# Kernel tuning notes

Hardware: AMD Instinct MI355X
Metric: run time of the kernel (lower is better)

## Reference

```python
import jax, jax.numpy as jnp
import numpy as np

T, IN, H, OUT, L = 2048, 128, 128, 128, 2


def setup_inputs() -> dict:
    key = jax.random.key(0)
    ks = jax.random.split(key, 12)
    s_in = 1.0 / np.sqrt(IN)
    s_h = 1.0 / np.sqrt(H)
    s_ff = 1.0 / np.sqrt(2 * H)
    return {
        "emb": jax.random.normal(ks[0], (T, IN), jnp.float32),
        "start": jax.random.randint(ks[1], (T,), 0, 2).astype(jnp.int32),
        "w_in": jax.random.normal(ks[2], (H, IN), jnp.float32) * s_in,
        "b_in": jnp.zeros((H,), jnp.float32),
        "w_out": jax.random.normal(ks[3], (OUT, H), jnp.float32) * s_h,
        "b_out": jnp.zeros((OUT,), jnp.float32),
        "w_f": jax.random.normal(ks[4], (L, 1, H), jnp.float32) * s_h,
        "b_f": jnp.zeros((L, 1), jnp.float32),
        "w_i": jax.random.normal(ks[5], (L, 1, H), jnp.float32) * s_h,
        "b_i": jnp.zeros((L, 1), jnp.float32),
        "w_v": jax.random.normal(ks[6], (L, H, H), jnp.float32) * s_h,
        "b_v": jnp.zeros((L, H), jnp.float32),
        "w_q": jax.random.normal(ks[7], (L, H, H), jnp.float32) * s_h,
        "b_q": jnp.zeros((L, H), jnp.float32),
        "w_k": jax.random.normal(ks[8], (L, H, H), jnp.float32) * s_h,
        "b_k": jnp.zeros((L, H), jnp.float32),
        "w_o": jax.random.normal(ks[9], (L, H, H), jnp.float32) * s_h,
        "b_o": jnp.zeros((L, H), jnp.float32),
        "w_ff": jax.random.normal(ks[10], (L, H, 2 * H), jnp.float32) * s_ff,
        "b_ff": jnp.zeros((L, H), jnp.float32),
    }


def _mlstm_layer(x, gate_mask, w_f, b_f, w_i, b_i, w_v, b_v, w_q, b_q, w_k, b_k, w_o, b_o):
    # x: [T, H] layer input; gate_mask: [T] (0.0 at episode starts -> reset)
    Hdim = x.shape[-1]
    i = jnp.exp(x @ w_i.T + b_i)                           # [T, 1] exp input gate
    v = x @ w_v.T + b_v                                    # [T, H]
    k = (x * (1.0 / np.sqrt(Hdim))) @ w_k.T + b_k          # [T, H] (1/sqrt(H) applied before Linear)
    C = i[:, :, None] * (v[:, :, None] * k[:, None, :])    # [T, H, H] gated outer products
    n = i * k                                              # [T, H]
    g = jax.nn.sigmoid(x @ w_f.T + b_f)[:, 0] * gate_mask  # [T] forget gate, zeroed at resets

    def step(carry, inp):
        S, m = carry
        Ct, nt, gt = inp
        S = gt * S + Ct
        m = gt * m + nt
        return (S, m), (S, m)

    init = (jnp.zeros((Hdim, Hdim), x.dtype), jnp.zeros((Hdim,), x.dtype))
    _, (S_all, m_all) = jax.lax.scan(step, init, (C, n, g))  # [T,H,H], [T,H]

    q = x @ w_q.T + b_q                                    # [T, H]
    o = jax.nn.sigmoid(x @ w_o.T + b_o)                    # [T, H]
    num = jnp.einsum('thk,tk->th', S_all, q)               # C @ q per step
    den = jnp.maximum(jnp.abs(jnp.einsum('th,th->t', m_all, q))[:, None], 1.0)
    return o * (num / den)


def reference(emb, start, w_in, b_in, w_out, b_out, w_f, b_f, w_i, b_i,
              w_v, b_v, w_q, b_q, w_k, b_k, w_o, b_o, w_ff, b_ff):
    gate_mask = 1.0 - start.astype(emb.dtype)              # reset => discard previous state
    e = emb @ w_in.T + b_in                                # [T, H]
    z = e
    for l in range(w_f.shape[0]):
        h = _mlstm_layer(z, gate_mask, w_f[l], b_f[l], w_i[l], b_i[l],
                         w_v[l], b_v[l], w_q[l], b_q[l], w_k[l], b_k[l], w_o[l], b_o[l])
        z = jax.nn.leaky_relu(jnp.concatenate([h, e], axis=-1) @ w_ff[l].T + b_ff[l])
    return z @ w_out.T + b_out
```

## Files before the change

kernel.cpp:

```cpp
#include <hip/hip_runtime.h>
#include <math.h>

#define TT 2048
#define HH 128
#define ROWS 8
#define SP 132
#define XR 144
#define NBLK (TT / ROWS)

__device__ __forceinline__ float dot4(float4 a, float4 b) {
    return a.x * b.x + a.y * b.y + a.z * b.z + a.w * b.w;
}

__device__ __forceinline__ int xidx(int r, int k) {
    return r * XR + ((k >> 5) * 36) + (k & 31);
}

__device__ __forceinline__ float2 load_f2_agent(const float* p) {
    unsigned long long u = __hip_atomic_load((const unsigned long long*)p,
                                             __ATOMIC_RELAXED, __HIP_MEMORY_SCOPE_AGENT);
    float2 r;
    r.x = __uint_as_float((unsigned)(u & 0xffffffffull));
    r.y = __uint_as_float((unsigned)(u >> 32));
    return r;
}
__device__ __forceinline__ float load_f_agent(const float* p) {
    return __hip_atomic_load(p, __ATOMIC_RELAXED, __HIP_MEMORY_SCOPE_AGENT);
}
__device__ __forceinline__ void store_f_agent(float* p, float v) {
    __hip_atomic_store(p, v, __ATOMIC_RELAXED, __HIP_MEMORY_SCOPE_AGENT);
}

__global__ __launch_bounds__(256) void prep_kernel(
        const float* __restrict__ w_in, const float* __restrict__ w_out,
        const float* __restrict__ w_v, const float* __restrict__ w_q,
        const float* __restrict__ w_k, const float* __restrict__ w_o,
        const float* __restrict__ w_ff,
        float4* __restrict__ win_p, float4* __restrict__ wout_p,
        float4* __restrict__ wcat, float4* __restrict__ wff_p,
        unsigned* __restrict__ bar) {
    int i = blockIdx.x * 256 + threadIdx.x;
    if (blockIdx.x == 0 && threadIdx.x < 16) bar[threadIdx.x] = 0u;
    if (i < 4096) {
        int cg = i >> 7, col = i & 127;
        win_p[i] = ((const float4*)w_in)[col * 32 + cg];
    } else if (i < 8192) {
        int j = i - 4096, cg = j >> 7, col = j & 127;
        wout_p[j] = ((const float4*)w_out)[col * 32 + cg];
    } else if (i < 40960) {
        int j = i - 8192;
        int l = j >> 14, r = j & 16383, cg = r >> 9, col = r & 511;
        int sel = col >> 7, cm = col & 127;
        const float* s = (sel == 0 ? w_v : sel == 1 ? w_q : sel == 2 ? w_k : w_o) + l * HH * HH;
        wcat[j] = ((const float4*)s)[cm * 32 + cg];
    } else {
        int j = i - 40960;
        int l = j >> 13, r = j & 8191, cg = r >> 7, col = r & 127;
        const float* s = w_ff + l * HH * 256;
        wff_p[j] = ((const float4*)s)[col * 64 + cg];
    }
}

__device__ __forceinline__ void grid_barrier(unsigned* __restrict__ ctr) {
    __syncthreads();
    if (threadIdx.x == 0) {
        atomicAdd(ctr, 1u);
        while (__hip_atomic_load(ctr, __ATOMIC_RELAXED, __HIP_MEMORY_SCOPE_AGENT)
               < (unsigned)NBLK) {
            __builtin_amdgcn_s_sleep(8);
        }
    }
    __syncthreads();
}

__device__ __forceinline__ void stage_wsh(const float4* __restrict__ src, float4* lds) {
    int tid = threadIdx.x;
    int wv = tid >> 6;
#pragma unroll
    for (int it = 0; it < 8; ++it) {
        __builtin_amdgcn_global_load_lds(
            (const __attribute__((address_space(1))) unsigned int*)(src + it * 1024 + tid),
            (__attribute__((address_space(3))) unsigned int*)(lds + it * 1024 + wv * 64),
            16, 0, 0);
    }
}

__device__ __forceinline__ void attn_row(int t0,
        const float* __restrict__ kb, const float* __restrict__ vb,
        const float* __restrict__ qs, const float* __restrict__ os,
        const float* __restrict__ g, const float* __restrict__ iexp,
        float* __restrict__ hs) {
    int tid = threadIdx.x;
    int wv = tid >> 6, lane = tid & 63;
    if (wv >= 8) return;
    int t = t0 + wv;
    float2 q2 = *(const float2*)(qs + wv * SP + 2 * lane);
    float2 o2 = *(const float2*)(os + wv * SP + 2 * lane);
    int tp = t;
    float2 k2 = load_f2_agent(kb + tp * HH + 2 * lane);
    float2 v2 = load_f2_agent(vb + tp * HH + 2 * lane);
    float ie = load_f_agent(iexp + tp), gv = load_f_agent(g + tp);
    float nx = 0.f, ny = 0.f, dsum = 0.f, decay = 1.f;
    while (true) {
        bool cont = (tp > 0) && (gv != 0.f);
        float2 k2n = {0.f, 0.f}, v2n = {0.f, 0.f};
        float ien = 0.f, gvn = 0.f;
        if (cont) {
            k2n = load_f2_agent(kb + (tp - 1) * HH + 2 * lane);
            v2n = load_f2_agent(vb + (tp - 1) * HH + 2 * lane);
            ien = load_f_agent(iexp + tp - 1); gvn = load_f_agent(g + tp - 1);
        }
        float p = k2.x * q2.x + k2.y * q2.y;
#pragma unroll
        for (int off = 1; off <= 32; off <<= 1) p += __shfl_xor(p, off, 64);
        float coeff = decay * ie * p;
        nx += coeff * v2.x; ny += coeff * v2.y; dsum += coeff;
        if (!cont) break;
        decay *= gv;
        tp--; k2 = k2n; v2 = v2n; ie = ien; gv = gvn;
    }
    float inv = 1.f / fmaxf(fabsf(dsum), 1.f);
    int d = 2 * lane;
    *(float2*)(hs + wv * XR + (d >> 5) * 36 + (d & 31)) =
        make_float2(o2.x * nx * inv, o2.y * ny * inv);
}

__device__ __forceinline__ void proj_fi(int t0, const float* __restrict__ xls,
        const float* __restrict__ w_f, const float* __restrict__ b_f,
        const float* __restrict__ w_i, const float* __restrict__ b_i,
        const int* __restrict__ start, float* __restrict__ g, float* __restrict__ iexp) {
    int tid = threadIdx.x;
    int wv = tid >> 6, lane = tid & 63;
    if (wv >= 8) return;
    int d = 2 * lane;
    float2 xv = *(const float2*)(xls + wv * XR + (d >> 5) * 36 + (d & 31));
    float pf = xv.x * w_f[d] + xv.y * w_f[d + 1];
    float pi = xv.x * w_i[d] + xv.y * w_i[d + 1];
#pragma unroll
    for (int off = 1; off <= 32; off <<= 1) {
        pf += __shfl_xor(pf, off, 64);
        pi += __shfl_xor(pi, off, 64);
    }
    if (lane == 0) {
        int t = t0 + wv;
        store_f_agent(g + t, start[t] ? 0.f : 1.f / (1.f + expf(-(pf + b_f[0]))));
        store_f_agent(iexp + t, expf(pi + b_i[0]));
    }
}

__device__ __forceinline__ void proj_block(int t0, const float* __restrict__ xls,
        const float4* __restrict__ wc,
        const float* __restrict__ b_v, const float* __restrict__ b_q,
        const float* __restrict__ b_k, const float* __restrict__ b_o,
        float* __restrict__ kb, float* __restrict__ vb,
        float* __restrict__ qs, float* __restrict__ os) {
    int tid = threadIdx.x;
    int lane = tid & 63, w = tid >> 6;
    int kc = lane >> 4, c = lane & 15;
    int cslot = (w & 7) * 16 + c;
    int mp = w >> 3;
    float a0[8] = {}, a1[8] = {};
#pragma unroll
    for (int j = 0; j < 8; ++j) {
        const float4* wb = wc + (kc * 8 + j) * 512 + mp * 256;
        float4 w0 = wb[cslot];
        float4 w1 = wb[128 + cslot];
#pragma unroll
        for (int rr = 0; rr < 8; ++rr) {
            float4 x4 = *(const float4*)(xls + rr * XR + kc * 36 + 4 * j);
            a0[rr] += dot4(x4, w0);
            a1[rr] += dot4(x4, w1);
        }
    }
#pragma unroll
    for (int rr = 0; rr < 8; ++rr) {
        a0[rr] += __shfl_xor(a0[rr], 16, 64); a0[rr] += __shfl_xor(a0[rr], 32, 64);
        a1[rr] += __shfl_xor(a1[rr], 16, 64); a1[rr] += __shfl_xor(a1[rr], 32, 64);
    }
    if (kc == 0) {
        if (mp == 0) {
            float bv = b_v[cslot], bq = b_q[cslot];
#pragma unroll
            for (int rr = 0; rr < 8; ++rr) {
                store_f_agent(vb + (t0 + rr) * HH + cslot, a0[rr] + bv);
                qs[rr * SP + cslot] = a1[rr] + bq;
            }
        } else {
            const float ks = 0.088388347648318447f;
            float bk = b_k[cslot], bo = b_o[cslot];
#pragma unroll
            for (int rr = 0; rr < 8; ++rr) {
                store_f_agent(kb + (t0 + rr) * HH + cslot, a0[rr] * ks + bk);
                os[rr * SP + cslot] = 1.f / (1.f + expf(-(a1[rr] + bo)));
            }
        }
    }
}

__device__ __forceinline__ void ff_block(const float* __restrict__ hsb,
        const float* __restrict__ esb, const float4* wffl,
        const float* __restrict__ b_ff, float* __restrict__ zs) {
    int tid = threadIdx.x;
    int lane = tid & 63, w = tid >> 6;
    int kc = lane >> 3, c = lane & 7;
    int col = (w >> 3) * 64 + (w & 7) * 8 + c;
    const float* xb = (kc < 4) ? hsb : esb;
    int coff = (kc & 3) * 36;
    float a0[8] = {};
#pragma unroll
    for (int j = 0; j < 8; ++j) {
        float4 w0 = wffl[(kc * 8 + j) * 128 + col];
#pragma unroll
        for (int rr = 0; rr < 8; ++rr) {
            float4 x4 = *(const float4*)(xb + rr * XR + coff + 4 * j);
            a0[rr] += dot4(x4, w0);
        }
    }
#pragma unroll
    for (int rr = 0; rr < 8; ++rr) {
        a0[rr] += __shfl_xor(a0[rr], 8, 64);
        a0[rr] += __shfl_xor(a0[rr], 16, 64);
        a0[rr] += __shfl_xor(a0[rr], 32, 64);
    }
    if (kc == 0) {
        float bb = b_ff[col];
#pragma unroll
        for (int rr = 0; rr < 8; ++rr) {
            float z = a0[rr] + bb;
            z = z > 0.f ? z : 0.01f * z;
            zs[xidx(rr, col)] = z;
        }
    }
}

__device__ __forceinline__ void dense128(int t0, const float* __restrict__ xls,
        const float4* __restrict__ Wp, const float* __restrict__ b,
        float* __restrict__ yg, float* __restrict__ ys) {
    int tid = threadIdx.x;
    int lane = tid & 63, w = tid >> 6;
    int kc = lane >> 3, c = lane & 7;
    int col = (w >> 3) * 64 + (w & 7) * 8 + c;
    float a0[8] = {};
#pragma unroll
    for (int j = 0; j < 4; ++j) {
        float4 w0 = Wp[(kc * 4 + j) * 128 + col];
        int off = (kc >> 1) * 36 + (kc & 1) * 16 + 4 * j;
#pragma unroll
        for (int rr = 0; rr < 8; ++rr) {
            float4 x4 = *(const float4*)(xls + rr * XR + off);
            a0[rr] += dot4(x4, w0);
        }
    }
#pragma unroll
    for (int rr = 0; rr < 8; ++rr) {
        a0[rr] += __shfl_xor(a0[rr], 8, 64);
        a0[rr] += __shfl_xor(a0[rr], 16, 64);
        a0[rr] += __shfl_xor(a0[rr], 32, 64);
    }
    if (kc == 0) {
        float bb = b[col];
#pragma unroll
        for (int rr = 0; rr < 8; ++rr) {
            float y = a0[rr] + bb;
            if (ys) ys[xidx(rr, col)] = y;
            if (yg) yg[(t0 + rr) * HH + col] = y;
        }
    }
}

__global__ __launch_bounds__(1024, 4) void mega_kernel(
        const float* __restrict__ emb, const int* __restrict__ start,
        const float4* __restrict__ win_p, const float* __restrict__ b_in,
        const float4* __restrict__ wcat,
        const float* __restrict__ b_v, const float* __restrict__ b_q,
        const float* __restrict__ b_k, const float* __restrict__ b_o,
        const float* __restrict__ w_f, const float* __restrict__ b_f,
        const float* __restrict__ w_i, const float* __restrict__ b_i,
        const float4* __restrict__ wff_p, const float* __restrict__ b_ff,
        const float4* __restrict__ wout_p, const float* __restrict__ b_out,
        float* __restrict__ k0b, float* __restrict__ v0b,
        float* __restrict__ k1b, float* __restrict__ v1b,
        float* __restrict__ g0, float* __restrict__ i0,
        float* __restrict__ g1, float* __restrict__ i1,
        unsigned* __restrict__ bar,
        float* __restrict__ out) {
    __shared__ float xs[ROWS * XR];
    __shared__ float es[ROWS * XR];
    __shared__ float hs[ROWS * XR];
    __shared__ float zs[ROWS * XR];
    __shared__ float qs[ROWS * SP];
    __shared__ float os[ROWS * SP];
    __shared__ float4 wsh[8192];
    int tid = threadIdx.x;
    int t0 = blockIdx.x * ROWS;

    {
        int row = tid >> 7, dd = tid & 127;
        xs[row * XR + (dd >> 5) * 36 + (dd & 31)] = emb[(t0 + row) * HH + dd];
    }
    __syncthreads();
    dense128(t0, xs, win_p, b_in, (float*)0, es);
    __syncthreads();
    proj_block(t0, es, wcat, b_v, b_q, b_k, b_o, k0b, v0b, qs, os);
    proj_fi(t0, es, w_f, b_f, w_i, b_i, start, g0, i0);
    grid_barrier(bar + 0);

    stage_wsh(wff_p, wsh);
    attn_row(t0, k0b, v0b, qs, os, g0, i0, hs);
    __syncthreads();
    ff_block(hs, es, wsh, b_ff, zs);
    __syncthreads();
    proj_block(t0, zs, wcat + 16384, b_v + HH, b_q + HH, b_k + HH, b_o + HH,
               k1b, v1b, qs, os);
    proj_fi(t0, zs, w_f + HH, b_f + 1, w_i + HH, b_i + 1, start, g1, i1);
    grid_barrier(bar + 1);

    stage_wsh(wff_p + 8192, wsh);
    attn_row(t0, k1b, v1b, qs, os, g1, i1, hs);
    __syncthreads();
    ff_block(hs, es, wsh, b_ff + HH, zs);
    __syncthreads();
    dense128(t0, zs, wout_p, b_out, out, (float*)0);
}

extern "C" void kernel_launch(void* const* d_in, const int* in_sizes, int n_in,
                              void* d_out, int out_size, void* d_ws, size_t ws_size,
                              hipStream_t stream) {
    const float* emb   = (const float*)d_in[0];
    const int*   start = (const int*)  d_in[1];
    const float* w_in  = (const float*)d_in[2];
    const float* b_in  = (const float*)d_in[3];
    const float* w_out = (const float*)d_in[4];
    const float* b_out = (const float*)d_in[5];
    const float* w_f   = (const float*)d_in[6];
    const float* b_f   = (const float*)d_in[7];
    const float* w_i   = (const float*)d_in[8];
    const float* b_i   = (const float*)d_in[9];
    const float* w_v   = (const float*)d_in[10];
    const float* b_v   = (const float*)d_in[11];
    const float* w_q   = (const float*)d_in[12];
    const float* b_q   = (const float*)d_in[13];
    const float* w_k   = (const float*)d_in[14];
    const float* b_k   = (const float*)d_in[15];
    const float* w_o   = (const float*)d_in[16];
    const float* b_o   = (const float*)d_in[17];
    const float* w_ff  = (const float*)d_in[18];
    const float* b_ff  = (const float*)d_in[19];
    float* out = (float*)d_out;

    unsigned* bar = (unsigned*)d_ws;
    float* ws = (float*)d_ws + 64;
    float* k0b = ws; ws += TT * HH;
    float* v0b = ws; ws += TT * HH;
    float* k1b = ws; ws += TT * HH;
    float* v1b = ws; ws += TT * HH;
    float* g0  = ws; ws += TT;
    float* i0  = ws; ws += TT;
    float* g1  = ws; ws += TT;
    float* i1  = ws; ws += TT;
    float4* win_p  = (float4*)ws; ws += 16384;
    float4* wout_p = (float4*)ws; ws += 16384;
    float4* wcat   = (float4*)ws; ws += 131072;
    float4* wff_p  = (float4*)ws; ws += 65536;

    prep_kernel<<<dim3(224), dim3(256), 0, stream>>>(
        w_in, w_out, w_v, w_q, w_k, w_o, w_ff, win_p, wout_p, wcat, wff_p, bar);
    mega_kernel<<<dim3(NBLK), dim3(1024), 0, stream>>>(
        emb, start, win_p, b_in, wcat,
        b_v, b_q, b_k, b_o, w_f, b_f, w_i, b_i,
        wff_p, b_ff, wout_p, b_out,
        k0b, v0b, k1b, v1b, g0, i0, g1, i1,
        bar, out);
}
```

Baseline: 141.7 us.

## Overlap attention scan with e-part of FF; precompute segment starts; batch history loads

Adds a prep pass that computes, for each timestep, the index of its episode start, so the attention loop knows its range in advance. The loop then loads four history steps at a time, letting loads overlap instead of chaining one prefetch per step. The FF matmul is split: warps 8-15, idle during attention, now compute the e-half contribution and stage only half of the FF weights. This halves the wsh LDS footprint, and the h-half is computed after the barrier. The extra prep blocks and the separate partial-sum buffer add small overhead.

```diff
diff --git a/kernel.cpp b/kernel.cpp
--- a/kernel.cpp
+++ b/kernel.cpp
@@ -35,10 +35,24 @@
         const float* __restrict__ w_in, const float* __restrict__ w_out,
         const float* __restrict__ w_v, const float* __restrict__ w_q,
         const float* __restrict__ w_k, const float* __restrict__ w_o,
-        const float* __restrict__ w_ff,
+        const float* __restrict__ w_ff, const int* __restrict__ start,
         float4* __restrict__ win_p, float4* __restrict__ wout_p,
         float4* __restrict__ wcat, float4* __restrict__ wff_p,
-        unsigned* __restrict__ bar) {
+        int* __restrict__ stb, unsigned* __restrict__ bar) {
+    if (blockIdx.x >= 224) {
+        __shared__ int sl[256];
+        int base = (blockIdx.x - 224) * 256;
+        int t = base + threadIdx.x;
+        sl[threadIdx.x] = start[t];
+        __syncthreads();
+        int s = t;
+        while (s > base && sl[s - base] == 0) --s;
+        if (s == base && sl[0] == 0) {
+            while (s > 0 && start[s] == 0) --s;
+        }
+        stb[t] = s;
+        return;
+    }
     int i = blockIdx.x * 256 + threadIdx.x;
     if (blockIdx.x == 0 && threadIdx.x < 16) bar[threadIdx.x] = 0u;
     if (i < 4096) {
@@ -73,51 +87,44 @@
     __syncthreads();
 }
 
-__device__ __forceinline__ void stage_wsh(const float4* __restrict__ src, float4* lds) {
-    int tid = threadIdx.x;
-    int wv = tid >> 6;
-#pragma unroll
-    for (int it = 0; it < 8; ++it) {
-        __builtin_amdgcn_global_load_lds(
-            (const __attribute__((address_space(1))) unsigned int*)(src + it * 1024 + tid),
-            (__attribute__((address_space(3))) unsigned int*)(lds + it * 1024 + wv * 64),
-            16, 0, 0);
-    }
-}
-
 __device__ __forceinline__ void attn_row(int t0,
         const float* __restrict__ kb, const float* __restrict__ vb,
         const float* __restrict__ qs, const float* __restrict__ os,
         const float* __restrict__ g, const float* __restrict__ iexp,
-        float* __restrict__ hs) {
+        const int* __restrict__ stb, float* __restrict__ hs) {
     int tid = threadIdx.x;
     int wv = tid >> 6, lane = tid & 63;
-    if (wv >= 8) return;
     int t = t0 + wv;
+    int st = stb[t];
     float2 q2 = *(const float2*)(qs + wv * SP + 2 * lane);
     float2 o2 = *(const float2*)(os + wv * SP + 2 * lane);
+    float nx = 0.f, ny = 0.f, dsum = 0.f, decay = 1.f;
     int tp = t;
-    float2 k2 = load_f2_agent(kb + tp * HH + 2 * lane);
-    float2 v2 = load_f2_agent(vb + tp * HH + 2 * lane);
-    float ie = load_f_agent(iexp + tp), gv = load_f_agent(g + tp);
-    float nx = 0.f, ny = 0.f, dsum = 0.f, decay = 1.f;
-    while (true) {
-        bool cont = (tp > 0) && (gv != 0.f);
-        float2 k2n = {0.f, 0.f}, v2n = {0.f, 0.f};
-        float ien = 0.f, gvn = 0.f;
-        if (cont) {
-            k2n = load_f2_agent(kb + (tp - 1) * HH + 2 * lane);
-            v2n = load_f2_agent(vb + (tp - 1) * HH + 2 * lane);
-            ien = load_f_agent(iexp + tp - 1); gvn = load_f_agent(g + tp - 1);
-        }
-        float p = k2.x * q2.x + k2.y * q2.y;
-#pragma unroll
-        for (int off = 1; off <= 32; off <<= 1) p += __shfl_xor(p, off, 64);
-        float coeff = decay * ie * p;
-        nx += coeff * v2.x; ny += coeff * v2.y; dsum += coeff;
-        if (!cont) break;
-        decay *= gv;
-        tp--; k2 = k2n; v2 = v2n; ie = ien; gv = gvn;
+    while (tp >= st) {
+        int nb = tp - st + 1; if (nb > 4) nb = 4;
+        float2 kk[4], vv[4];
+        float ie[4], gv[4];
+#pragma unroll
+        for (int b = 0; b < 4; ++b) {
+            if (b < nb) {
+                kk[b] = load_f2_agent(kb + (tp - b) * HH + 2 * lane);
+                vv[b] = load_f2_agent(vb + (tp - b) * HH + 2 * lane);
+                ie[b] = load_f_agent(iexp + (tp - b));
+                gv[b] = load_f_agent(g + (tp - b));
+            }
+        }
+#pragma unroll
+        for (int b = 0; b < 4; ++b) {
+            if (b < nb) {
+                float p = kk[b].x * q2.x + kk[b].y * q2.y;
+#pragma unroll
+                for (int off = 1; off <= 32; off <<= 1) p += __shfl_xor(p, off, 64);
+                float coeff = decay * ie[b] * p;
+                nx += coeff * vv[b].x; ny += coeff * vv[b].y; dsum += coeff;
+                if (tp - b > st) decay *= gv[b];
+            }
+        }
+        tp -= nb;
     }
     float inv = 1.f / fmaxf(fabsf(dsum), 1.f);
     int d = 2 * lane;
@@ -197,22 +204,83 @@
     }
 }
 
-__device__ __forceinline__ void ff_block(const float* __restrict__ hsb,
-        const float* __restrict__ esb, const float4* wffl,
+__device__ __forceinline__ void ffe_block(const float* __restrict__ esb,
+        const float4* __restrict__ wffg, float* __restrict__ zp) {
+    int tid = threadIdx.x;
+    int lane = tid & 63, w = tid >> 6;
+    int kc = lane >> 4, c = lane & 15;
+    int cslot = (w - 8) * 16 + c;
+    float acc[8] = {};
+#pragma unroll
+    for (int j = 0; j < 8; ++j) {
+        float4 w0 = wffg[(32 + kc * 8 + j) * 128 + cslot];
+#pragma unroll
+        for (int rr = 0; rr < 8; ++rr) {
+            float4 x4 = *(const float4*)(esb + rr * XR + kc * 36 + 4 * j);
+            acc[rr] += dot4(x4, w0);
+        }
+    }
+#pragma unroll
+    for (int rr = 0; rr < 8; ++rr) {
+        acc[rr] += __shfl_xor(acc[rr], 16, 64);
+        acc[rr] += __shfl_xor(acc[rr], 32, 64);
+    }
+    if (kc == 0) {
+#pragma unroll
+        for (int rr = 0; rr < 8; ++rr) zp[rr * SP + cslot] = acc[rr];
+    }
+}
+
+__device__ __forceinline__ void ffh_block(const float* __restrict__ hsb,
+        const float4* wshl, const float* __restrict__ zp,
         const float* __restrict__ b_ff, float* __restrict__ zs) {
+    int tid = threadIdx.x;
+    int lane = tid & 63, w = tid >> 6;
+    int kc = lane >> 4, c = lane & 15;
+    int rg = w >> 3;
+    int cslot = (w & 7) * 16 + c;
+    float acc[4] = {};
+#pragma unroll
+    for (int j = 0; j < 8; ++j) {
+        float4 w0 = wshl[(kc * 8 + j) * 128 + cslot];
+#pragma unroll
+        for (int rr = 0; rr < 4; ++rr) {
+            float4 x4 = *(const float4*)(hsb + (rg * 4 + rr) * XR + kc * 36 + 4 * j);
+            acc[rr] += dot4(x4, w0);
+        }
+    }
+#pragma unroll
+    for (int rr = 0; rr < 4; ++rr) {
+        acc[rr] += __shfl_xor(acc[rr], 16, 64);
+        acc[rr] += __shfl_xor(acc[rr], 32, 64);
+    }
+    if (kc == 0) {
+        float bb = b_ff[cslot];
+#pragma unroll
+        for (int rr = 0; rr < 4; ++rr) {
+            int r = rg * 4 + rr;
+            float z = acc[rr] + zp[r * SP + cslot] + bb;
+            z = z > 0.f ? z : 0.01f * z;
+            zs[xidx(r, cslot)] = z;
+        }
+    }
+}
+
+__device__ __forceinline__ void dense128(int t0, const float* __restrict__ xls,
+        const float4* __restrict__ Wp, const float* __restrict__ b,
+        float* __restrict__ yg, float* __restrict__ ys) {
     int tid = threadIdx.x;
     int lane = tid & 63, w = tid >> 6;
     int kc = lane >> 3, c = lane & 7;
     int col = (w >> 3) * 64 + (w & 7) * 8 + c;
-    const float* xb = (kc < 4) ? hsb : esb;
-    int coff = (kc & 3) * 36;
     float a0[8] = {};
 #pragma unroll
-    for (int j = 0; j < 8; ++j) {
-        float4 w0 = wffl[(kc * 8 + j) * 128 + col];
+    for (int j = 0; j < 4; ++j) {
+        float4 w0 = Wp[(kc * 4 + j) * 128 + col];
+        int off = (kc >> 1) * 36 + (kc & 1) * 16 + 4 * j;
 #pragma unroll
         for (int rr = 0; rr < 8; ++rr) {
-            float4 x4 = *(const float4*)(xb + rr * XR + coff + 4 * j);
+            float4 x4 = *(const float4*)(xls + rr * XR + off);
             a0[rr] += dot4(x4, w0);
         }
     }
@@ -223,41 +291,6 @@
         a0[rr] += __shfl_xor(a0[rr], 32, 64);
     }
     if (kc == 0) {
-        float bb = b_ff[col];
-#pragma unroll
-        for (int rr = 0; rr < 8; ++rr) {
-            float z = a0[rr] + bb;
-            z = z > 0.f ? z : 0.01f * z;
-            zs[xidx(rr, col)] = z;
-        }
-    }
-}
-
-__device__ __forceinline__ void dense128(int t0, const float* __restrict__ xls,
-        const float4* __restrict__ Wp, const float* __restrict__ b,
-        float* __restrict__ yg, float* __restrict__ ys) {
-    int tid = threadIdx.x;
-    int lane = tid & 63, w = tid >> 6;
-    int kc = lane >> 3, c = lane & 7;
-    int col = (w >> 3) * 64 + (w & 7) * 8 + c;
-    float a0[8] = {};
-#pragma unroll
-    for (int j = 0; j < 4; ++j) {
-        float4 w0 = Wp[(kc * 4 + j) * 128 + col];
-        int off = (kc >> 1) * 36 + (kc & 1) * 16 + 4 * j;
-#pragma unroll
-        for (int rr = 0; rr < 8; ++rr) {
-            float4 x4 = *(const float4*)(xls + rr * XR + off);
-            a0[rr] += dot4(x4, w0);
-        }
-    }
-#pragma unroll
-    for (int rr = 0; rr < 8; ++rr) {
-        a0[rr] += __shfl_xor(a0[rr], 8, 64);
-        a0[rr] += __shfl_xor(a0[rr], 16, 64);
-        a0[rr] += __shfl_xor(a0[rr], 32, 64);
-    }
-    if (kc == 0) {
         float bb = b[col];
 #pragma unroll
         for (int rr = 0; rr < 8; ++rr) {
@@ -265,6 +298,18 @@
             if (ys) ys[xidx(rr, col)] = y;
             if (yg) yg[(t0 + rr) * HH + col] = y;
         }
+    }
+}
+
+__device__ __forceinline__ void stage_wsh_h(const float4* __restrict__ src, float4* lds) {
+    int tid2 = threadIdx.x - 512;
+    int wv2 = tid2 >> 6;
+#pragma unroll
+    for (int it = 0; it < 8; ++it) {
+        __builtin_amdgcn_global_load_lds(
+            (const __attribute__((address_space(1))) unsigned int*)(src + it * 512 + tid2),
+            (__attribute__((address_space(3))) unsigned int*)(lds + it * 512 + wv2 * 64),
+            16, 0, 0);
     }
 }
 
@@ -282,7 +327,7 @@
         float* __restrict__ k1b, float* __restrict__ v1b,
         float* __restrict__ g0, float* __restrict__ i0,
         float* __restrict__ g1, float* __restrict__ i1,
-        unsigned* __restrict__ bar,
+        const int* __restrict__ stb, unsigned* __restrict__ bar,
         float* __restrict__ out) {
     __shared__ float xs[ROWS * XR];
     __shared__ float es[ROWS * XR];
@@ -290,9 +335,11 @@
     __shared__ float zs[ROWS * XR];
     __shared__ float qs[ROWS * SP];
     __shared__ float os[ROWS * SP];
-    __shared__ float4 wsh[8192];
+    __shared__ float zp[ROWS * SP];
+    __shared__ float4 wsh[4096];
     int tid = threadIdx.x;
     int t0 = blockIdx.x * ROWS;
+    int wv = tid >> 6;
 
     {
         int row = tid >> 7, dd = tid & 127;
@@ -305,20 +352,28 @@
     proj_fi(t0, es, w_f, b_f, w_i, b_i, start, g0, i0);
     grid_barrier(bar + 0);
 
-    stage_wsh(wff_p, wsh);
-    attn_row(t0, k0b, v0b, qs, os, g0, i0, hs);
-    __syncthreads();
-    ff_block(hs, es, wsh, b_ff, zs);
+    if (wv < 8) {
+        attn_row(t0, k0b, v0b, qs, os, g0, i0, stb, hs);
+    } else {
+        stage_wsh_h(wff_p, wsh);
+        ffe_block(es, wff_p, zp);
+    }
+    __syncthreads();
+    ffh_block(hs, wsh, zp, b_ff, zs);
     __syncthreads();
     proj_block(t0, zs, wcat + 16384, b_v + HH, b_q + HH, b_k + HH, b_o + HH,
                k1b, v1b, qs, os);
     proj_fi(t0, zs, w_f + HH, b_f + 1, w_i + HH, b_i + 1, start, g1, i1);
     grid_barrier(bar + 1);
 
-    stage_wsh(wff_p + 8192, wsh);
-    attn_row(t0, k1b, v1b, qs, os, g1, i1, hs);
-    __syncthreads();
-    ff_block(hs, es, wsh, b_ff + HH, zs);
+    if (wv < 8) {
+        attn_row(t0, k1b, v1b, qs, os, g1, i1, stb, hs);
+    } else {
+        stage_wsh_h(wff_p + 8192, wsh);
+        ffe_block(es, wff_p + 8192, zp);
+    }
+    __syncthreads();
+    ffh_block(hs, wsh, zp, b_ff + HH, zs);
     __syncthreads();
     dense128(t0, zs, wout_p, b_out, out, (float*)0);
 }
@@ -358,17 +413,19 @@
     float* i0  = ws; ws += TT;
     float* g1  = ws; ws += TT;
     float* i1  = ws; ws += TT;
+    int* stb   = (int*)ws; ws += TT;
     float4* win_p  = (float4*)ws; ws += 16384;
     float4* wout_p = (float4*)ws; ws += 16384;
     float4* wcat   = (float4*)ws; ws += 131072;
     float4* wff_p  = (float4*)ws; ws += 65536;
 
-    prep_kernel<<<dim3(224), dim3(256), 0, stream>>>(
-        w_in, w_out, w_v, w_q, w_k, w_o, w_ff, win_p, wout_p, wcat, wff_p, bar);
+    prep_kernel<<<dim3(232), dim3(256), 0, stream>>>(
+        w_in, w_out, w_v, w_q, w_k, w_o, w_ff, start,
+        win_p, wout_p, wcat, wff_p, stb, bar);
     mega_kernel<<<dim3(NBLK), dim3(1024), 0, stream>>>(
         emb, start, win_p, b_in, wcat,
         b_v, b_q, b_k, b_o, w_f, b_f, w_i, b_i,
         wff_p, b_ff, wout_p, b_out,
         k0b, v0b, k1b, v1b, g0, i0, g1, i1,
-        bar, out);
-}
+        stb, bar, out);
+}
```

Result: faster. 138.0 us (-2.6%).
